# Optimization experiments

Hardware: AMD Instinct MI355X
Metric: run time of the kernel (lower is better)

Reference implementation:

```python
import jax, jax.numpy as jnp
import numpy as np

TOP_N = 0.15  # ResultsErasing(top_n=0.15) and MCPA self.ratio usage


def setup_inputs() -> dict:
    key = jax.random.key(0)
    k1, k2, k3 = jax.random.split(key, 3)
    N, C, H, W = 16, 9, 512, 512
    inp = jax.random.normal(k1, (N, C, H, W), dtype=jnp.float32)   # net1 logits
    x = jax.random.normal(k2, (N, 1, H, W), dtype=jnp.float32)     # raw image
    ratio = jax.random.uniform(k3, (N,), dtype=jnp.float32)        # per-sample erase ratio
    return {"inp": inp, "x": x, "ratio": ratio}


def reference(inp, x, ratio):
    """ResultsErasing: per-(sample,channel) top-k threshold, scatter-zero mask.

    torch semantics:
      f_p  = int(ratio[n] * H * W)
      k    = int(f_p * TOP_N)                  # same k for every channel of sample n
      thr  = k-th largest of inp[n, c]         (thr = 1 if k == 0)
      x2[n, :][inp[n, c] > thr] = 0  for every channel c  -> OR over channels
    """
    N, C, H, W = inp.shape
    HW = H * W
    flat = inp.reshape(N, C, HW)
    sorted_desc = -jnp.sort(-flat, axis=-1)                      # [N, C, HW] descending
    f_p = jnp.floor(ratio * HW)                                  # int(ratio[n]*H*W)
    k = jnp.floor(f_p * TOP_N).astype(jnp.int32)                 # [N]
    idx = jnp.clip(k - 1, 0, HW - 1)[:, None, None]              # [N,1,1]
    thr = jnp.take_along_axis(sorted_desc, jnp.broadcast_to(idx, (N, C, 1)), axis=-1)[..., 0]  # [N,C]
    thr = jnp.where(k[:, None] == 0, jnp.asarray(1.0, inp.dtype), thr)
    # OR over input channels: any logit channel above its threshold erases the pixel
    mask = jnp.any(flat > thr[:, :, None], axis=1).reshape(N, 1, H, W)
    return jnp.where(mask, jnp.zeros((), x.dtype), x)
```

## Files before the change

### kernel.cpp

```cpp
#include <hip/hip_runtime.h>
#include <stdint.h>

#define NS 16
#define CHN 9
#define NC 144
#define HW 262144
#define HW4 65536
#define HIST_STRIDE 1024
#define OVER_BIN 896u
#define PREF_LO 0xBE80u

#define OFF_HIST 0
#define OFF_META 147456
#define OFF_BMP  147888

__device__ __forceinline__ unsigned fkey(float f) {
  unsigned u = __float_as_uint(f);
  unsigned m = (unsigned)((int)u >> 31) | 0x80000000u;
  return u ^ m;
}

__global__ void k_zero(unsigned* __restrict__ ws, int n) {
  int i = blockIdx.x * 256 + threadIdx.x;
  if (i < n) ws[i] = 0u;
}

__global__ __launch_bounds__(256) void k_hist(const float* __restrict__ inp,
                                              unsigned* __restrict__ hist) {
  __shared__ unsigned lh[HIST_STRIDE];
  int plane = blockIdx.x >> 4;
  int sub = blockIdx.x & 15;
  for (int i = threadIdx.x; i < HIST_STRIDE; i += 256) lh[i] = 0u;
  __syncthreads();
  unsigned spread = 897u + (threadIdx.x & 31u);
  const float4* base = (const float4*)inp + (size_t)plane * HW4 + (size_t)sub * 4096;
#pragma unroll
  for (int it = 0; it < 16; it += 8) {
    float4 v[8];
#pragma unroll
    for (int j = 0; j < 8; ++j) v[j] = base[(it + j) * 256 + threadIdx.x];
#pragma unroll
    for (int j = 0; j < 8; ++j) {
      float e[4] = {v[j].x, v[j].y, v[j].z, v[j].w};
#pragma unroll
      for (int q = 0; q < 4; ++q) {
        unsigned bin = (fkey(e[q]) >> 16) - PREF_LO;
        bin = (bin < OVER_BIN) ? bin : ((bin < 0x8000u) ? OVER_BIN : spread);
        atomicAdd(&lh[bin], 1u);
      }
    }
  }
  __syncthreads();
  unsigned* gh = hist + plane * HIST_STRIDE;
  for (int i = threadIdx.x; i < HIST_STRIDE; i += 256) {
    unsigned c = lh[i];
    if (c) atomicAdd(&gh[i], c);
  }
}

__global__ __launch_bounds__(256) void k_scan(const unsigned* __restrict__ hist,
                                              const float* __restrict__ ratio,
                                              unsigned* __restrict__ meta) {
  int ch = blockIdx.x;
  int t = threadIdx.x;
  unsigned* Dm = meta;
  unsigned* Pm = meta + NC;
  unsigned* Km = meta + 2 * NC;
  float r = ratio[ch / CHN];
  float fp = floorf(r * 262144.0f);
  int k = (int)floorf(fp * 0.15f);
  if (k <= 0) {
    if (t == 0) { Dm[ch] = 0xBF800000u;
                  Pm[ch] = 0xFFFFFFFFu; Km[ch] = 0u; }
    return;
  }
  const unsigned* h = hist + ch * HIST_STRIDE;
  unsigned b0 = h[4 * t], b1 = h[4 * t + 1], b2 = h[4 * t + 2], b3 = h[4 * t + 3];
  if (4 * t + 0 > 896) b0 = 0;
  if (4 * t + 1 > 896) b1 = 0;
  if (4 * t + 2 > 896) b2 = 0;
  if (4 * t + 3 > 896) b3 = 0;
  unsigned s = b0 + b1 + b2 + b3;
  __shared__ unsigned incl[256];
  incl[t] = s;
  __syncthreads();
  for (int off = 1; off < 256; off <<= 1) {
    unsigned add = (t + off < 256) ? incl[t + off] : 0u;
    __syncthreads();
    incl[t] += add;
    __syncthreads();
  }
  unsigned above = (t < 255) ? incl[t + 1] : 0u;
  unsigned uk = (unsigned)k;
  if (incl[t] >= uk && above < uk) {
    unsigned bins[4] = {b0, b1, b2, b3};
    unsigned cum = above;
    for (int j = 3; j >= 0; --j) {
      unsigned c = bins[j];
      if (cum + c >= uk) {
        int b = 4 * t + j;
        if (b >= (int)OVER_BIN) {
          Dm[ch] = 0xFFFFFFFFu; Pm[ch] = 0xFFFFFFFFu; Km[ch] = 0u;
        } else {
          unsigned pref = PREF_LO + (unsigned)b;
          Dm[ch] = (pref << 16) | 0xFFFFu;
          Pm[ch] = pref;
          Km[ch] = uk - cum;
        }
        break;
      }
      cum += c;
    }
  }
}

__global__ __launch_bounds__(256) void k_mask(const float* __restrict__ inp,
                                              const float* __restrict__ x,
                                              const unsigned* __restrict__ meta,
                                              unsigned long long* __restrict__ bmp,
                                              float* __restrict__ out) {
  int b = blockIdx.x;
  int n = b >> 8;
  int p4 = ((b & 255) << 8) + threadIdx.x;
  const unsigned* Dm = meta;
  const unsigned* Pm = meta + NC;
  int lane = threadIdx.x & 63;
  size_t wbase = (size_t)(b & 255) * 4 + (threadIdx.x >> 6);

  float4 xv = ((const float4*)x)[(size_t)n * HW4 + p4];
  float4 v[CHN];
#pragma unroll
  for (int c = 0; c < CHN; ++c)
    v[c] = ((const float4*)inp)[(size_t)(n * CHN + c) * HW4 + p4];

  unsigned m0 = 0u, m1 = 0u, m2 = 0u, m3 = 0u;
#pragma unroll
  for (int c = 0; c < CHN; ++c) {
    int ch = n * CHN + c;
    unsigned D = Dm[ch], P = Pm[ch];
    unsigned k0 = fkey(v[c].x), k1 = fkey(v[c].y), k2 = fkey(v[c].z), k3 = fkey(v[c].w);
    m0 |= (k0 > D); m1 |= (k1 > D); m2 |= (k2 > D); m3 |= (k3 > D);
    bool isc = ((k0 >> 16) == P) | ((k1 >> 16) == P) |
               ((k2 >> 16) == P) | ((k3 >> 16) == P);
    unsigned long long bal = __ballot(isc);
    if (lane == 0) bmp[(size_t)ch * 1024 + wbase] = bal;
  }
  float4 ov;
  ov.x = m0 ? 0.0f : xv.x;
  ov.y = m1 ? 0.0f : xv.y;
  ov.z = m2 ? 0.0f : xv.z;
  ov.w = m3 ? 0.0f : xv.w;
  ((float4*)out)[(size_t)n * HW4 + p4] = ov;
}

__global__ __launch_bounds__(256) void k_resolve(const float* __restrict__ inp,
                                                 const unsigned* __restrict__ meta,
                                                 const unsigned long long* __restrict__ bmp,
                                                 float* __restrict__ out) {
  int ch = blockIdx.x;
  unsigned P = meta[NC + ch];
  if (P == 0xFFFFFFFFu) return;
  unsigned kp = meta[2 * NC + ch];
  int n = ch / CHN;
  __shared__ unsigned s_grp[4096];
  __shared__ unsigned s_pix[4096];
  __shared__ unsigned short s_lo[4096];
  __shared__ unsigned h[256];
  __shared__ unsigned s_ng, s_nc, s_hb, s_kpp, s_thr;
  if (threadIdx.x == 0) { s_ng = 0u; s_nc = 0u; }
  __syncthreads();
  const unsigned long long* w = bmp + (size_t)ch * 1024;
  for (int i = threadIdx.x; i < 1024; i += 256) {
    unsigned long long word = w[i];
    while (word) {
      int bit = __ffsll((long long)word) - 1;
      unsigned idx = atomicAdd(&s_ng, 1u);
      if (idx < 4096u) s_grp[idx] = (unsigned)(i * 64 + bit);
      word &= word - 1;
    }
  }
  __syncthreads();
  unsigned ng = min(s_ng, 4096u);
  for (unsigned i = threadIdx.x; i < ng; i += 256) {
    unsigned g = s_grp[i];
    float4 v = ((const float4*)inp)[(size_t)ch * HW4 + g];
    unsigned kk[4] = {fkey(v.x), fkey(v.y), fkey(v.z), fkey(v.w)};
#pragma unroll
    for (int j = 0; j < 4; ++j) {
      if ((kk[j] >> 16) == P) {
        unsigned idx = atomicAdd(&s_nc, 1u);
        if (idx < 4096u) {
          s_pix[idx] = g * 4 + (unsigned)j;
          s_lo[idx] = (unsigned short)(kk[j] & 0xFFFFu);
        }
      }
    }
  }
  __syncthreads();
  unsigned cnt = min(s_nc, 4096u);
  h[threadIdx.x] = 0u;
  __syncthreads();
  for (unsigned i = threadIdx.x; i < cnt; i += 256) atomicAdd(&h[s_lo[i] >> 8], 1u);
  __syncthreads();
  if (threadIdx.x == 0) {
    unsigned cum = 0, hb = 0, kk2 = kp;
    for (int b2 = 255; b2 >= 0; --b2) {
      unsigned c = h[b2];
      if (cum + c >= kp) { hb = (unsigned)b2; kk2 = kp - cum; break; }
      cum += c;
    }
    s_hb = hb; s_kpp = kk2;
  }
  __syncthreads();
  unsigned hb = s_hb, kpp = s_kpp;
  h[threadIdx.x] = 0u;
  __syncthreads();
  for (unsigned i = threadIdx.x; i < cnt; i += 256) {
    unsigned l = s_lo[i];
    if ((l >> 8) == hb) atomicAdd(&h[l & 0xFFu], 1u);
  }
  __syncthreads();
  if (threadIdx.x == 0) {
    unsigned cum = 0, lb = 0;
    for (int b2 = 255; b2 >= 0; --b2) {
      unsigned c = h[b2];
      if (cum + c >= kpp) { lb = (unsigned)b2; break; }
      cum += c;
    }
    s_thr = (hb << 8) | lb;
  }
  __syncthreads();
  unsigned thr_lo = s_thr;
  for (unsigned i = threadIdx.x; i < cnt; i += 256) {
    if ((unsigned)s_lo[i] > thr_lo) out[(size_t)n * HW + s_pix[i]] = 0.0f;
  }
}

extern "C" void kernel_launch(void* const* d_in, const int* in_sizes, int n_in,
                              void* d_out, int out_size, void* d_ws, size_t ws_size,
                              hipStream_t stream) {
  (void)in_sizes; (void)n_in; (void)out_size; (void)ws_size;
  const float* inp = (const float*)d_in[0];
  const float* x = (const float*)d_in[1];
  const float* ratio = (const float*)d_in[2];
  float* out = (float*)d_out;
  unsigned* ws = (unsigned*)d_ws;

  unsigned* hist = ws + OFF_HIST;
  unsigned* meta = ws + OFF_META;
  unsigned long long* bmp = (unsigned long long*)(ws + OFF_BMP);

  int zn = OFF_META;
  k_zero<<<(zn + 255) / 256, 256, 0, stream>>>(ws, zn);
  k_hist<<<NC * 16, 256, 0, stream>>>(inp, hist);
  k_scan<<<NC, 256, 0, stream>>>(hist, ratio, meta);
  k_mask<<<NS * 256, 256, 0, stream>>>(inp, x, meta, bmp, out);
  k_resolve<<<NC, 256, 0, stream>>>(inp, meta, bmp, out);
}
```

Before: 288.6 us.

## Restructure top-k threshold pipeline with per-plane byte masks and separate apply pass

The histogram now only bins keys at or above the float 1.0 key range (385 bins), so values below the lowest possible threshold skip the shared atomics. The mask kernel is split per plane and writes a byte per float4 holding definite and candidate bits instead of ballot bitmaps and the output. The resolve kernel radix-selects the exact threshold over candidate keys and ORs bits into the byte mask, and a new apply kernel ORs the nine channel masks and writes the output. This trades an extra pass and a byte-mask buffer (about 9.4MB written and read) for fewer histogram atomics and no scattered writes to the output.

```diff
diff --git a/kernel.cpp b/kernel.cpp
--- a/kernel.cpp
+++ b/kernel.cpp
@@ -6,13 +6,17 @@
 #define NC 144
 #define HW 262144
 #define HW4 65536
-#define HIST_STRIDE 1024
-#define OVER_BIN 896u
-#define PREF_LO 0xBE80u
+#define KEY1 0xBF800000u
+#define NBIN 385
+#define PREF0 0xBF80u
+#define HSTRIDE 512
+#define RCAP 8192
 
 #define OFF_HIST 0
-#define OFF_META 147456
-#define OFF_BMP  147888
+#define OFF_MC   73728
+#define OFF_MD   73872
+#define OFF_MK   74016
+#define OFF_BYTES 74160
 
 __device__ __forceinline__ unsigned fkey(float f) {
   unsigned u = __float_as_uint(f);
@@ -20,39 +24,35 @@
   return u ^ m;
 }
 
-__global__ void k_zero(unsigned* __restrict__ ws, int n) {
-  int i = blockIdx.x * 256 + threadIdx.x;
-  if (i < n) ws[i] = 0u;
-}
-
 __global__ __launch_bounds__(256) void k_hist(const float* __restrict__ inp,
                                               unsigned* __restrict__ hist) {
-  __shared__ unsigned lh[HIST_STRIDE];
+  __shared__ unsigned lh[HSTRIDE];
   int plane = blockIdx.x >> 4;
   int sub = blockIdx.x & 15;
-  for (int i = threadIdx.x; i < HIST_STRIDE; i += 256) lh[i] = 0u;
-  __syncthreads();
-  unsigned spread = 897u + (threadIdx.x & 31u);
+  for (int i = threadIdx.x; i < HSTRIDE; i += 256) lh[i] = 0u;
+  __syncthreads();
   const float4* base = (const float4*)inp + (size_t)plane * HW4 + (size_t)sub * 4096;
 #pragma unroll
-  for (int it = 0; it < 16; it += 8) {
+  for (int chunk = 0; chunk < 2; ++chunk) {
     float4 v[8];
 #pragma unroll
-    for (int j = 0; j < 8; ++j) v[j] = base[(it + j) * 256 + threadIdx.x];
+    for (int j = 0; j < 8; ++j) v[j] = base[(chunk * 8 + j) * 256 + threadIdx.x];
 #pragma unroll
     for (int j = 0; j < 8; ++j) {
       float e[4] = {v[j].x, v[j].y, v[j].z, v[j].w};
 #pragma unroll
       for (int q = 0; q < 4; ++q) {
-        unsigned bin = (fkey(e[q]) >> 16) - PREF_LO;
-        bin = (bin < OVER_BIN) ? bin : ((bin < 0x8000u) ? OVER_BIN : spread);
-        atomicAdd(&lh[bin], 1u);
+        unsigned key = fkey(e[q]);
+        if (key >= KEY1) {
+          unsigned bin = min((key >> 16) - PREF0, (unsigned)(NBIN - 1));
+          atomicAdd(&lh[bin], 1u);
+        }
       }
     }
   }
   __syncthreads();
-  unsigned* gh = hist + plane * HIST_STRIDE;
-  for (int i = threadIdx.x; i < HIST_STRIDE; i += 256) {
+  unsigned* gh = hist + plane * HSTRIDE;
+  for (int i = threadIdx.x; i < HSTRIDE; i += 256) {
     unsigned c = lh[i];
     if (c) atomicAdd(&gh[i], c);
   }
@@ -60,29 +60,21 @@
 
 __global__ __launch_bounds__(256) void k_scan(const unsigned* __restrict__ hist,
                                               const float* __restrict__ ratio,
-                                              unsigned* __restrict__ meta) {
+                                              unsigned* __restrict__ metaC,
+                                              unsigned* __restrict__ metaD,
+                                              unsigned* __restrict__ metaK) {
   int ch = blockIdx.x;
   int t = threadIdx.x;
-  unsigned* Dm = meta;
-  unsigned* Pm = meta + NC;
-  unsigned* Km = meta + 2 * NC;
   float r = ratio[ch / CHN];
   float fp = floorf(r * 262144.0f);
   int k = (int)floorf(fp * 0.15f);
-  if (k <= 0) {
-    if (t == 0) { Dm[ch] = 0xBF800000u;
-                  Pm[ch] = 0xFFFFFFFFu; Km[ch] = 0u; }
-    return;
-  }
-  const unsigned* h = hist + ch * HIST_STRIDE;
-  unsigned b0 = h[4 * t], b1 = h[4 * t + 1], b2 = h[4 * t + 2], b3 = h[4 * t + 3];
-  if (4 * t + 0 > 896) b0 = 0;
-  if (4 * t + 1 > 896) b1 = 0;
-  if (4 * t + 2 > 896) b2 = 0;
-  if (4 * t + 3 > 896) b3 = 0;
-  unsigned s = b0 + b1 + b2 + b3;
+  if (t == 0) { metaC[ch] = KEY1 + 1u; metaD[ch] = KEY1 + 1u; metaK[ch] = 0u; }
+  __syncthreads();
+  if (k <= 0) return;
+  const unsigned* h = hist + ch * HSTRIDE;
+  unsigned h0 = h[2 * t], h1 = h[2 * t + 1];
   __shared__ unsigned incl[256];
-  incl[t] = s;
+  incl[t] = h0 + h1;
   __syncthreads();
   for (int off = 1; off < 256; off <<= 1) {
     unsigned add = (t + off < 256) ? incl[t + off] : 0u;
@@ -93,146 +85,143 @@
   unsigned above = (t < 255) ? incl[t + 1] : 0u;
   unsigned uk = (unsigned)k;
   if (incl[t] >= uk && above < uk) {
-    unsigned bins[4] = {b0, b1, b2, b3};
     unsigned cum = above;
-    for (int j = 3; j >= 0; --j) {
-      unsigned c = bins[j];
-      if (cum + c >= uk) {
-        int b = 4 * t + j;
-        if (b >= (int)OVER_BIN) {
-          Dm[ch] = 0xFFFFFFFFu; Pm[ch] = 0xFFFFFFFFu; Km[ch] = 0u;
-        } else {
-          unsigned pref = PREF_LO + (unsigned)b;
-          Dm[ch] = (pref << 16) | 0xFFFFu;
-          Pm[ch] = pref;
-          Km[ch] = uk - cum;
-        }
-        break;
+    int B;
+    if (cum + h1 >= uk) { B = 2 * t + 1; }
+    else { cum += h1; B = 2 * t; }
+    if (B >= NBIN - 1) {
+      metaC[ch] = 0xC1000000u; metaD[ch] = 0xFFFFFFFFu;
+    } else {
+      unsigned pref = PREF0 + (unsigned)B;
+      metaC[ch] = pref << 16; metaD[ch] = (pref + 1u) << 16;
+    }
+    metaK[ch] = uk - cum;
+  }
+}
+
+__global__ __launch_bounds__(256) void k_mask(const float* __restrict__ inp,
+                                              const unsigned* __restrict__ metaC,
+                                              const unsigned* __restrict__ metaD,
+                                              unsigned char* __restrict__ bytes) {
+  int plane = blockIdx.x >> 4;
+  int sub = blockIdx.x & 15;
+  unsigned C = metaC[plane], D = metaD[plane];
+  const float4* base = (const float4*)inp + (size_t)plane * HW4 + (size_t)sub * 4096;
+  unsigned char* ob = bytes + (size_t)plane * HW4 + (size_t)sub * 4096;
+#pragma unroll
+  for (int chunk = 0; chunk < 2; ++chunk) {
+    float4 v[8];
+#pragma unroll
+    for (int j = 0; j < 8; ++j) v[j] = base[(chunk * 8 + j) * 256 + threadIdx.x];
+#pragma unroll
+    for (int j = 0; j < 8; ++j) {
+      unsigned k0 = fkey(v[j].x), k1 = fkey(v[j].y), k2 = fkey(v[j].z), k3 = fkey(v[j].w);
+      unsigned def = (unsigned)(k0 >= D) | ((unsigned)(k1 >= D) << 1) |
+                     ((unsigned)(k2 >= D) << 2) | ((unsigned)(k3 >= D) << 3);
+      unsigned gec = (unsigned)(k0 >= C) | ((unsigned)(k1 >= C) << 1) |
+                     ((unsigned)(k2 >= C) << 2) | ((unsigned)(k3 >= C) << 3);
+      unsigned cnd = gec & ~def;
+      ob[(chunk * 8 + j) * 256 + threadIdx.x] = (unsigned char)(def | (cnd << 4));
+    }
+  }
+}
+
+__global__ __launch_bounds__(256) void k_resolve(const float* __restrict__ inp,
+                                                 const unsigned* __restrict__ metaC,
+                                                 const unsigned* __restrict__ metaD,
+                                                 const unsigned* __restrict__ metaK,
+                                                 unsigned* __restrict__ defcand_w) {
+  int ch = blockIdx.x;
+  unsigned C = metaC[ch], D = metaD[ch];
+  if (C == D) return;
+  unsigned kp = metaK[ch];
+  __shared__ unsigned s_pos[RCAP];
+  __shared__ unsigned s_key[RCAP];
+  __shared__ unsigned h[256];
+  __shared__ unsigned s_nc, s_chosen, s_kr;
+  if (threadIdx.x == 0) { s_nc = 0u; s_chosen = 0u; s_kr = kp; }
+  __syncthreads();
+  const uint4* w4 = (const uint4*)(defcand_w + ((size_t)ch << 14));
+  for (int i = threadIdx.x; i < 4096; i += 256) {
+    uint4 w = w4[i];
+    unsigned ws_[4] = {w.x, w.y, w.z, w.w};
+#pragma unroll
+    for (int s = 0; s < 4; ++s) {
+      unsigned m = ws_[s] & 0xF0F0F0F0u;
+      int gb = i * 16 + s * 4;
+      while (m) {
+        int bit = __ffs(m) - 1;
+        int byteI = bit >> 3;
+        int q = (bit & 7) - 4;
+        unsigned idx = atomicAdd(&s_nc, 1u);
+        if (idx < (unsigned)RCAP) s_pos[idx] = (unsigned)((gb + byteI) * 4 + q);
+        m &= m - 1u;
       }
-      cum += c;
-    }
-  }
-}
-
-__global__ __launch_bounds__(256) void k_mask(const float* __restrict__ inp,
-                                              const float* __restrict__ x,
-                                              const unsigned* __restrict__ meta,
-                                              unsigned long long* __restrict__ bmp,
-                                              float* __restrict__ out) {
-  int b = blockIdx.x;
-  int n = b >> 8;
-  int p4 = ((b & 255) << 8) + threadIdx.x;
-  const unsigned* Dm = meta;
-  const unsigned* Pm = meta + NC;
-  int lane = threadIdx.x & 63;
-  size_t wbase = (size_t)(b & 255) * 4 + (threadIdx.x >> 6);
-
-  float4 xv = ((const float4*)x)[(size_t)n * HW4 + p4];
-  float4 v[CHN];
+    }
+  }
+  __syncthreads();
+  unsigned cnt = min(s_nc, (unsigned)RCAP);
+  for (unsigned i = threadIdx.x; i < cnt; i += 256)
+    s_key[i] = fkey(inp[((size_t)ch << 18) + s_pos[i]]);
+  __syncthreads();
+  for (int lev = 3; lev >= 0; --lev) {
+    h[threadIdx.x] = 0u;
+    __syncthreads();
+    int sh = lev * 8;
+    unsigned himask = (lev == 3) ? 0u : (0xFFFFFFFFu << (sh + 8));
+    unsigned chosen = s_chosen;
+    for (unsigned i = threadIdx.x; i < cnt; i += 256) {
+      unsigned key = s_key[i];
+      if ((key & himask) == chosen) atomicAdd(&h[(key >> sh) & 0xFFu], 1u);
+    }
+    __syncthreads();
+    if (threadIdx.x == 0) {
+      unsigned kr = s_kr, cum = 0u, cb = 0u;
+      for (int b = 255; b >= 0; --b) {
+        unsigned c = h[b];
+        if (cum + c >= kr) { cb = (unsigned)b; s_kr = kr - cum; break; }
+        cum += c;
+      }
+      s_chosen = chosen | (cb << sh);
+    }
+    __syncthreads();
+  }
+  unsigned thr_key = s_chosen;
+  for (unsigned i = threadIdx.x; i < cnt; i += 256) {
+    if (s_key[i] > thr_key) {
+      unsigned pos = s_pos[i];
+      unsigned g = pos >> 2;
+      unsigned q = pos & 3u;
+      unsigned word = (((unsigned)ch << 16) + g) >> 2;
+      atomicOr(&defcand_w[word], (1u << q) << (8u * (g & 3u)));
+    }
+  }
+}
+
+__global__ __launch_bounds__(256) void k_apply(const float* __restrict__ x,
+                                               const unsigned* __restrict__ defcand_w,
+                                               float* __restrict__ out) {
+  int t = blockIdx.x * 256 + threadIdx.x;
+  int n = t >> 14;
+  int wi = t & 16383;
+  unsigned orw = 0u;
 #pragma unroll
   for (int c = 0; c < CHN; ++c)
-    v[c] = ((const float4*)inp)[(size_t)(n * CHN + c) * HW4 + p4];
-
-  unsigned m0 = 0u, m1 = 0u, m2 = 0u, m3 = 0u;
-#pragma unroll
-  for (int c = 0; c < CHN; ++c) {
-    int ch = n * CHN + c;
-    unsigned D = Dm[ch], P = Pm[ch];
-    unsigned k0 = fkey(v[c].x), k1 = fkey(v[c].y), k2 = fkey(v[c].z), k3 = fkey(v[c].w);
-    m0 |= (k0 > D); m1 |= (k1 > D); m2 |= (k2 > D); m3 |= (k3 > D);
-    bool isc = ((k0 >> 16) == P) | ((k1 >> 16) == P) |
-               ((k2 >> 16) == P) | ((k3 >> 16) == P);
-    unsigned long long bal = __ballot(isc);
-    if (lane == 0) bmp[(size_t)ch * 1024 + wbase] = bal;
-  }
-  float4 ov;
-  ov.x = m0 ? 0.0f : xv.x;
-  ov.y = m1 ? 0.0f : xv.y;
-  ov.z = m2 ? 0.0f : xv.z;
-  ov.w = m3 ? 0.0f : xv.w;
-  ((float4*)out)[(size_t)n * HW4 + p4] = ov;
-}
-
-__global__ __launch_bounds__(256) void k_resolve(const float* __restrict__ inp,
-                                                 const unsigned* __restrict__ meta,
-                                                 const unsigned long long* __restrict__ bmp,
-                                                 float* __restrict__ out) {
-  int ch = blockIdx.x;
-  unsigned P = meta[NC + ch];
-  if (P == 0xFFFFFFFFu) return;
-  unsigned kp = meta[2 * NC + ch];
-  int n = ch / CHN;
-  __shared__ unsigned s_grp[4096];
-  __shared__ unsigned s_pix[4096];
-  __shared__ unsigned short s_lo[4096];
-  __shared__ unsigned h[256];
-  __shared__ unsigned s_ng, s_nc, s_hb, s_kpp, s_thr;
-  if (threadIdx.x == 0) { s_ng = 0u; s_nc = 0u; }
-  __syncthreads();
-  const unsigned long long* w = bmp + (size_t)ch * 1024;
-  for (int i = threadIdx.x; i < 1024; i += 256) {
-    unsigned long long word = w[i];
-    while (word) {
-      int bit = __ffsll((long long)word) - 1;
-      unsigned idx = atomicAdd(&s_ng, 1u);
-      if (idx < 4096u) s_grp[idx] = (unsigned)(i * 64 + bit);
-      word &= word - 1;
-    }
-  }
-  __syncthreads();
-  unsigned ng = min(s_ng, 4096u);
-  for (unsigned i = threadIdx.x; i < ng; i += 256) {
-    unsigned g = s_grp[i];
-    float4 v = ((const float4*)inp)[(size_t)ch * HW4 + g];
-    unsigned kk[4] = {fkey(v.x), fkey(v.y), fkey(v.z), fkey(v.w)};
-#pragma unroll
-    for (int j = 0; j < 4; ++j) {
-      if ((kk[j] >> 16) == P) {
-        unsigned idx = atomicAdd(&s_nc, 1u);
-        if (idx < 4096u) {
-          s_pix[idx] = g * 4 + (unsigned)j;
-          s_lo[idx] = (unsigned short)(kk[j] & 0xFFFFu);
-        }
-      }
-    }
-  }
-  __syncthreads();
-  unsigned cnt = min(s_nc, 4096u);
-  h[threadIdx.x] = 0u;
-  __syncthreads();
-  for (unsigned i = threadIdx.x; i < cnt; i += 256) atomicAdd(&h[s_lo[i] >> 8], 1u);
-  __syncthreads();
-  if (threadIdx.x == 0) {
-    unsigned cum = 0, hb = 0, kk2 = kp;
-    for (int b2 = 255; b2 >= 0; --b2) {
-      unsigned c = h[b2];
-      if (cum + c >= kp) { hb = (unsigned)b2; kk2 = kp - cum; break; }
-      cum += c;
-    }
-    s_hb = hb; s_kpp = kk2;
-  }
-  __syncthreads();
-  unsigned hb = s_hb, kpp = s_kpp;
-  h[threadIdx.x] = 0u;
-  __syncthreads();
-  for (unsigned i = threadIdx.x; i < cnt; i += 256) {
-    unsigned l = s_lo[i];
-    if ((l >> 8) == hb) atomicAdd(&h[l & 0xFFu], 1u);
-  }
-  __syncthreads();
-  if (threadIdx.x == 0) {
-    unsigned cum = 0, lb = 0;
-    for (int b2 = 255; b2 >= 0; --b2) {
-      unsigned c = h[b2];
-      if (cum + c >= kpp) { lb = (unsigned)b2; break; }
-      cum += c;
-    }
-    s_thr = (hb << 8) | lb;
-  }
-  __syncthreads();
-  unsigned thr_lo = s_thr;
-  for (unsigned i = threadIdx.x; i < cnt; i += 256) {
-    if ((unsigned)s_lo[i] > thr_lo) out[(size_t)n * HW + s_pix[i]] = 0.0f;
+    orw |= defcand_w[(((size_t)(n * CHN + c)) << 14) + wi];
+  const float4* xp = (const float4*)x + (((size_t)n) << 16) + (size_t)wi * 4;
+  float4* op = (float4*)out + (((size_t)n) << 16) + (size_t)wi * 4;
+  float4 xv[4];
+#pragma unroll
+  for (int j = 0; j < 4; ++j) xv[j] = xp[j];
+#pragma unroll
+  for (int j = 0; j < 4; ++j) {
+    unsigned bits = (orw >> (8 * j)) & 0xFu;
+    float4 ov;
+    ov.x = (bits & 1u) ? 0.0f : xv[j].x;
+    ov.y = (bits & 2u) ? 0.0f : xv[j].y;
+    ov.z = (bits & 4u) ? 0.0f : xv[j].z;
+    ov.w = (bits & 8u) ? 0.0f : xv[j].w;
+    op[j] = ov;
   }
 }
 
@@ -247,13 +236,16 @@
   unsigned* ws = (unsigned*)d_ws;
 
   unsigned* hist = ws + OFF_HIST;
-  unsigned* meta = ws + OFF_META;
-  unsigned long long* bmp = (unsigned long long*)(ws + OFF_BMP);
-
-  int zn = OFF_META;
-  k_zero<<<(zn + 255) / 256, 256, 0, stream>>>(ws, zn);
+  unsigned* metaC = ws + OFF_MC;
+  unsigned* metaD = ws + OFF_MD;
+  unsigned* metaK = ws + OFF_MK;
+  unsigned* defcand_w = ws + OFF_BYTES;
+  unsigned char* defcand_b = (unsigned char*)defcand_w;
+
+  hipMemsetAsync(hist, 0, (size_t)NC * HSTRIDE * 4, stream);
   k_hist<<<NC * 16, 256, 0, stream>>>(inp, hist);
-  k_scan<<<NC, 256, 0, stream>>>(hist, ratio, meta);
-  k_mask<<<NS * 256, 256, 0, stream>>>(inp, x, meta, bmp, out);
-  k_resolve<<<NC, 256, 0, stream>>>(inp, meta, bmp, out);
-}
+  k_scan<<<NC, 256, 0, stream>>>(hist, ratio, metaC, metaD, metaK);
+  k_mask<<<NC * 16, 256, 0, stream>>>(inp, metaC, metaD, defcand_b);
+  k_resolve<<<NC, 256, 0, stream>>>(inp, metaC, metaD, metaK, defcand_w);
+  k_apply<<<1024, 256, 0, stream>>>(x, defcand_w, out);
+}
```

New measurement: 334.9 us. +16.1%, slower.
